# Optimization experiments

Measured on AMD Instinct MI355X. Metric: run time of the kernel, lower is better.

## Reference

```python
import jax, jax.numpy as jnp
import numpy as np

N, E = 10000, 160000
HID, EDIM = 256, 128
EPS = 1e-5


def _layernorm(x, g, b):
    mu = jnp.mean(x, axis=-1, keepdims=True)
    var = jnp.mean(jnp.square(x - mu), axis=-1, keepdims=True)
    return (x - mu) * jax.lax.rsqrt(var + EPS) * g + b


def setup_inputs() -> dict:
    key = jax.random.key(0)
    ks = jax.random.split(key, 12)
    cat_dim = 2 * HID + EDIM  # 640

    def lin(k, fan_in, fan_out):
        kw, kb = jax.random.split(k)
        lim = 1.0 / np.sqrt(fan_in)
        W = jax.random.uniform(kw, (fan_in, fan_out), jnp.float32, -lim, lim)
        b = jax.random.uniform(kb, (fan_out,), jnp.float32, -lim, lim)
        return W, b

    We1, be1 = lin(ks[0], cat_dim, EDIM)
    We2, be2 = lin(ks[1], EDIM, EDIM)
    Wv1, bv1 = lin(ks[2], cat_dim, HID)
    Wv2, bv2 = lin(ks[3], HID, HID)

    return {
        "h": jax.random.normal(ks[4], (N, HID), jnp.float32),
        "e": jax.random.normal(ks[5], (E, EDIM), jnp.float32),
        "edge_index": jax.random.randint(ks[6], (2, E), 0, N, jnp.int64),
        "We1": We1, "be1": be1, "We2": We2, "be2": be2,
        "Wv1": Wv1, "bv1": bv1, "Wv2": Wv2, "bv2": bv2,
        "ne_g": jnp.ones((EDIM,), jnp.float32), "ne_b": jnp.zeros((EDIM,), jnp.float32),
        "nv_g": jnp.ones((HID,), jnp.float32), "nv_b": jnp.zeros((HID,), jnp.float32),
    }


def reference(h, e, edge_index, We1, be1, We2, be2, Wv1, bv1, Wv2, bv2,
              ne_g, ne_b, nv_g, nv_b):
    # Eval mode: dropout and edge_drop are identity.
    src, dst = edge_index[0], edge_index[1]
    h_src = h[src]  # [E, HID] gather
    h_dst = h[dst]  # [E, HID] gather

    # Edge update: phi_e(concat) -> residual + LayerNorm
    xe = jnp.concatenate([h_src, h_dst, e], axis=-1)  # [E, 2H+ED]
    e_msg = jax.nn.gelu(xe @ We1 + be1, approximate=False) @ We2 + be2
    e_new = _layernorm(e + e_msg, ne_g, ne_b)

    # Node update: phi_v(concat with updated e) -> scatter_mean -> residual + LN
    xv = jnp.concatenate([h_src, h_dst, e_new], axis=-1)
    m = jax.nn.gelu(xv @ Wv1 + bv1, approximate=False) @ Wv2 + bv2  # [E, HID]
    agg = jax.ops.segment_sum(m, dst, num_segments=h.shape[0])
    counts = jax.ops.segment_sum(jnp.ones((m.shape[0], 1), m.dtype), dst,
                                 num_segments=h.shape[0])
    agg = agg / jnp.maximum(counts, 1.0)
    h_new = _layernorm(h + agg, nv_g, nv_b)
    return (h_new, e_new)
```

## Files before the change

kernel.cpp:

```cpp
#include <hip/hip_runtime.h>
#include <hip/hip_bf16.h>

#define NNODE 10000
#define NEDGE 160000
#define HIDD  256
#define ED    128
#define CAT   640

typedef short bf8 __attribute__((ext_vector_type(8)));
typedef short bf4 __attribute__((ext_vector_type(4)));
typedef float f4  __attribute__((ext_vector_type(4)));
typedef unsigned int u32;

__device__ __forceinline__ float bf2f(ushort u) {
    return __uint_as_float(((unsigned)u) << 16);
}
__device__ __forceinline__ ushort f2bf(float f) {
    unsigned u = __float_as_uint(f);
    return (ushort)((u + 0x7fffu + ((u >> 16) & 1u)) >> 16);
}
__device__ __forceinline__ float gelu_fast(float x) {
    float x2 = x * x;
    float u = 0.7978845608028654f * x * (1.0f + 0.044715f * x2);
    float au = fabsf(u);
    float ex = __expf(2.0f * au);
    float t = 1.0f - 2.0f / (1.0f + ex);
    t = copysignf(t, u);
    return 0.5f * x * (1.0f + t);
}
__device__ __forceinline__ int clampi(int v) {
    return ((unsigned)v >= (unsigned)NNODE) ? 0 : v;
}
__device__ __forceinline__ int getidx(const int* ei, bool i64, int pos) {
    int v = i64 ? ei[2 * pos] : ei[pos];
    return clampi(v);
}
__device__ __forceinline__ float loadf(const void* p, size_t idx, bool f32) {
    return f32 ? ((const float*)p)[idx] : bf2f(((const ushort*)p)[idx]);
}
__device__ __forceinline__ bf8 load8(const void* p, size_t idx, bool f32) {
    if (f32) {
        const float* fp = (const float*)p + idx;
        f4 lo = *(const f4*)fp, hi = *(const f4*)(fp + 4);
        bf8 r;
        r[0] = (short)f2bf(lo[0]); r[1] = (short)f2bf(lo[1]);
        r[2] = (short)f2bf(lo[2]); r[3] = (short)f2bf(lo[3]);
        r[4] = (short)f2bf(hi[0]); r[5] = (short)f2bf(hi[1]);
        r[6] = (short)f2bf(hi[2]); r[7] = (short)f2bf(hi[3]);
        return r;
    }
    return *(const bf8*)((const ushort*)p + idx);
}
__device__ __forceinline__ void storef(void* p, size_t idx, float v, bool f32) {
    if (f32) ((float*)p)[idx] = v;
    else     ((ushort*)p)[idx] = f2bf(v);
}
__device__ __forceinline__ void fadd_native(float* p, float v) {
    unsafeAtomicAdd(p, v);
}

__global__ void detect_kernel(const u32* __restrict__ h_u32,
                              const u32* __restrict__ ei_u32,
                              u32* __restrict__ flags) {
    int t = threadIdx.x;
    u32 e8 = (h_u32[t] >> 7) & 0xFFu;
    bool inw = (e8 >= 100u && e8 <= 150u);
    unsigned long long m = __ballot(inw);
    bool hi_nz = (t < 16) ? (ei_u32[2 * t + 1] != 0u) : false;
    unsigned long long m2 = __ballot(hi_nz);
    if (t == 0) {
        flags[0] = (__popcll(m) < 40) ? 1u : 0u;
        flags[1] = (m2 == 0ull) ? 1u : 0u;
    }
}

__global__ void prep_kernel(const void* __restrict__ We1, const void* __restrict__ We2,
                            const void* __restrict__ Wv1, const void* __restrict__ Wv2,
                            ushort* __restrict__ WT, const u32* __restrict__ flags) {
    const bool f32 = flags[0] != 0;
    int idx = blockIdx.x * 256 + threadIdx.x;
    if (idx >= 327680) return;
    const void* W; int base, k0, K, Wld;
    if      (idx <  32768) { W = We1; base = 0;      k0 = 0;   K = 256; Wld = 128; }
    else if (idx <  65536) { W = We1; base = 32768;  k0 = 256; K = 256; Wld = 128; }
    else if (idx <  81920) { W = We1; base = 65536;  k0 = 512; K = 128; Wld = 128; }
    else if (idx <  98304) { W = We2; base = 81920;  k0 = 0;   K = 128; Wld = 128; }
    else if (idx < 163840) { W = Wv1; base = 98304;  k0 = 0;   K = 256; Wld = 256; }
    else if (idx < 229376) { W = Wv1; base = 163840; k0 = 256; K = 256; Wld = 256; }
    else if (idx < 262144) { W = Wv1; base = 229376; k0 = 512; K = 128; Wld = 256; }
    else                   { W = Wv2; base = 262144; k0 = 0;   K = 256; Wld = 256; }
    int local = idx - base;
    int k = local & (K - 1);
    int n = local / K;
    WT[idx] = f2bf(loadf(W, (size_t)(k0 + k) * Wld + n, f32));
}

__global__ void hconv_kernel(const void* __restrict__ h, ushort* __restrict__ hb,
                             const u32* __restrict__ flags) {
    const bool f32 = flags[0] != 0;
    int i = blockIdx.x * 256 + threadIdx.x;
    if (i < NNODE * HIDD / 8)
        *(bf8*)&hb[(size_t)i * 8] = load8(h, (size_t)i * 8, f32);
}

__global__ void count_kernel(const int* __restrict__ ei, u32* __restrict__ cnt,
                             const u32* __restrict__ flags) {
    bool i64 = flags[1] != 0;
    int i = blockIdx.x * 256 + threadIdx.x;
    if (i < NEDGE) atomicAdd(&cnt[getidx(ei, i64, NEDGE + i)], 1u);
}

__global__ void scan_kernel(const u32* __restrict__ cnt, int* __restrict__ head) {
    __shared__ u32 part[256];
    __shared__ u32 base[256];
    int t = threadIdx.x;
    u32 s = 0;
    for (int j = 0; j < 40; ++j) {
        int i = t * 40 + j;
        if (i < NNODE) s += cnt[i];
    }
    part[t] = s;
    __syncthreads();
    if (t == 0) {
        u32 run = 0;
        for (int i = 0; i < 256; ++i) { base[i] = run; run += part[i]; }
    }
    __syncthreads();
    u32 run = base[t];
    for (int j = 0; j < 40; ++j) {
        int i = t * 40 + j;
        if (i < NNODE) { head[i] = (int)run; run += cnt[i]; }
    }
}

__global__ void fill_kernel(const int* __restrict__ ei, int* __restrict__ head,
                            int* __restrict__ perm, int* __restrict__ dsts,
                            const u32* __restrict__ flags) {
    bool i64 = flags[1] != 0;
    int i = blockIdx.x * 256 + threadIdx.x;
    if (i < NEDGE) {
        int d = getidx(ei, i64, NEDGE + i);
        int pos = atomicAdd(&head[d], 1);
        perm[pos] = i;
        dsts[pos] = d;
    }
}

template<int NB>
__device__ __forceinline__ void qp_body(const ushort* __restrict__ hb,
                                        const ushort* __restrict__ WT,
                                        const void* __restrict__ bias,
                                        ushort* __restrict__ O, int bid, bool f32) {
    const int tid = threadIdx.x;
    const int wid = tid >> 6, lane = tid & 63;
    const int l16 = lane & 15, lg = lane >> 4;
    const int node0 = bid * 64;
    const int N = NB * 64;
    const int n0 = wid * (NB * 16);

    size_t ra[4];
    #pragma unroll
    for (int ai = 0; ai < 4; ++ai) {
        int row = node0 + ai * 16 + l16;
        ra[ai] = (size_t)(row < NNODE ? row : NNODE - 1) * HIDD;
    }
    int bb[NB];
    #pragma unroll
    for (int bi = 0; bi < NB; ++bi) bb[bi] = (n0 + bi * 16 + l16) * HIDD;

    f4 acc[4][NB] = {};
    for (int kc = 0; kc < 4; ++kc) {
        #pragma unroll
        for (int ks = 0; ks < 2; ++ks) {
            int kk = kc * 64 + ks * 32 + lg * 8;
            bf8 b[NB];
            #pragma unroll
            for (int bi = 0; bi < NB; ++bi) b[bi] = *(const bf8*)&WT[bb[bi] + kk];
            #pragma unroll
            for (int ai = 0; ai < 4; ++ai) {
                bf8 a = *(const bf8*)&hb[ra[ai] + kk];
                #pragma unroll
                for (int bi = 0; bi < NB; ++bi)
                    acc[ai][bi] = __builtin_amdgcn_mfma_f32_16x16x32_bf16(a, b[bi], acc[ai][bi], 0, 0, 0);
            }
        }
    }
    #pragma unroll
    for (int bi = 0; bi < NB; ++bi) {
        int col = n0 + bi * 16 + l16;
        int pcol; float badd;
        if constexpr (NB == 4) {
            int hh = col >> 7, c = col & 127;
            badd = (hh == 0) ? loadf(bias, c, f32) : 0.f;
            pcol = hh * 128 + (c & 15) * 8 + (c >> 4);
        } else {
            int hh = col >> 8, c = col & 255;
            badd = (hh == 0) ? loadf(bias, c, f32) : 0.f;
            int nh2 = c >> 7, rem = c & 127, w = rem >> 5, b2 = (rem >> 4) & 1, l = c & 15;
            pcol = hh * 256 + w * 64 + l * 4 + nh2 * 2 + b2;
        }
        #pragma unroll
        for (int ai = 0; ai < 4; ++ai)
            #pragma unroll
            for (int r = 0; r < 4; ++r) {
                int gr = node0 + ai * 16 + lg * 4 + r;
                if (gr < NNODE) O[(size_t)gr * N + pcol] = f2bf(acc[ai][bi][r] + badd);
            }
    }
}

#define QPB ((NNODE + 63) / 64)
__global__ __launch_bounds__(256) void qp2_kernel(
    const ushort* __restrict__ hb, const ushort* __restrict__ WTe,
    const ushort* __restrict__ WTv, const void* __restrict__ be1,
    const void* __restrict__ bv1, ushort* __restrict__ Qab,
    ushort* __restrict__ Pab, const u32* __restrict__ flags) {
    const bool f32 = flags[0] != 0;
    if (blockIdx.x < QPB) qp_body<4>(hb, WTe, be1, Qab, blockIdx.x, f32);
    else                  qp_body<8>(hb, WTv, bv1, Pab, blockIdx.x - QPB, f32);
}

#define FWG (NEDGE / 128)
__global__ __launch_bounds__(512) void fused_kernel(
    const void* __restrict__ e, const int* __restrict__ ei,
    const int* __restrict__ perm, const int* __restrict__ dsts,
    const ushort* __restrict__ WT1c,
    const ushort* __restrict__ WT2, const void* __restrict__ be2,
    const ushort* __restrict__ Qab,
    const void* __restrict__ neg, const void* __restrict__ neb,
    const ushort* __restrict__ WvcT,
    const ushort* __restrict__ Pab,
    float* __restrict__ S, void* __restrict__ out,
    const u32* __restrict__ flags)
{
    const bool f32 = flags[0] != 0, i64 = flags[1] != 0;
    __shared__ ushort Asm[128 * 72];
    __shared__ ushort Bsm[128 * 72];
    __shared__ ushort Tsm[128 * 136];
    __shared__ int PermS[128], SrcS[128], DstS[128];

    int orig = blockIdx.x;
    int xcd = orig & 7, slot = orig >> 3;
    int bid = (xcd < 2 ? xcd * 157 : 2 * 157 + (xcd - 2) * 156) + slot;

    const int tid = threadIdx.x;
    const int wid = tid >> 6, lane = tid & 63;
    const int l16 = lane & 15, lg = lane >> 4;
    const int edge0 = bid * 128;
    const int rm = wid * 16;

    if (tid < 128) {
        int eid = perm[edge0 + tid];
        PermS[tid] = eid;
        SrcS[tid] = getidx(ei, i64, eid);
        DstS[tid] = dsts[edge0 + tid];
    }
    __syncthreads();

    f4 acc[8] = {};
    for (int kc = 0; kc < 2; ++kc) {
        __syncthreads();
        #pragma unroll
        for (int half = 0; half < 2; ++half) {
            int slot2 = tid + half * 512;
            int r = slot2 >> 3, c8 = (slot2 & 7) * 8;
            int eid = PermS[r];
            *(bf8*)&Asm[r * 72 + c8] = load8(e, (size_t)eid * ED + kc * 64 + c8, f32);
        }
        #pragma unroll
        for (int it = 0; it < 2; ++it) {
            int slot2 = tid + it * 512;
            int n = slot2 >> 3, c8 = (slot2 & 7) * 8;
            *(bf8*)&Bsm[n * 72 + c8] = *(const bf8*)&WT1c[n * 128 + kc * 64 + c8];
        }
        __syncthreads();
        #pragma unroll
        for (int ks = 0; ks < 2; ++ks) {
            bf8 a = *(const bf8*)&Asm[(rm + l16) * 72 + ks * 32 + lg * 8];
            #pragma unroll
            for (int f = 0; f < 8; ++f) {
                bf8 b = *(const bf8*)&Bsm[(f * 16 + l16) * 72 + ks * 32 + lg * 8];
                acc[f] = __builtin_amdgcn_mfma_f32_16x16x32_bf16(a, b, acc[f], 0, 0, 0);
            }
        }
    }

    {
        int sidx[4], didx[4];
        #pragma unroll
        for (int r = 0; r < 4; ++r) {
            int row = rm + lg * 4 + r;
            sidx[r] = SrcS[row];
            didx[r] = DstS[row];
        }
        bf8 qs[4], qd[4];
        #pragma unroll
        for (int r = 0; r < 4; ++r) {
            qs[r] = *(const bf8*)&Qab[(size_t)sidx[r] * 256 + l16 * 8];
            qd[r] = *(const bf8*)&Qab[(size_t)didx[r] * 256 + 128 + l16 * 8];
        }
        #pragma unroll
        for (int f = 0; f < 8; ++f) {
            #pragma unroll
            for (int r = 0; r < 4; ++r) {
                float val = acc[f][r] + bf2f((ushort)qs[r][f]) + bf2f((ushort)qd[r][f]);
                Tsm[(rm + lg * 4 + r) * 136 + f * 16 + l16] = f2bf(gelu_fast(val));
            }
        }
    }

    f4 acc2[8] = {};
    for (int kc = 0; kc < 2; ++kc) {
        __syncthreads();
        #pragma unroll
        for (int it = 0; it < 2; ++it) {
            int slot2 = tid + it * 512;
            int n = slot2 >> 3, c8 = (slot2 & 7) * 8;
            *(bf8*)&Bsm[n * 72 + c8] = *(const bf8*)&WT2[n * 128 + kc * 64 + c8];
        }
        __syncthreads();
        #pragma unroll
        for (int ks = 0; ks < 2; ++ks) {
            bf8 a = *(const bf8*)&Tsm[(rm + l16) * 136 + kc * 64 + ks * 32 + lg * 8];
            #pragma unroll
            for (int f = 0; f < 8; ++f) {
                bf8 b = *(const bf8*)&Bsm[(f * 16 + l16) * 72 + ks * 32 + lg * 8];
                acc2[f] = __builtin_amdgcn_mfma_f32_16x16x32_bf16(a, b, acc2[f], 0, 0, 0);
            }
        }
    }

    {
        float v[8][4];
        #pragma unroll
        for (int f = 0; f < 8; ++f) {
            int col = f * 16 + l16;
            float bias = loadf(be2, col, f32);
            #pragma unroll
            for (int r = 0; r < 4; ++r) {
                int row = rm + lg * 4 + r;
                v[f][r] = acc2[f][r] + bias
                        + loadf(e, (size_t)PermS[row] * ED + col, f32);
            }
        }
        #pragma unroll
        for (int r = 0; r < 4; ++r) {
            float s = 0.f;
            #pragma unroll
            for (int f = 0; f < 8; ++f) s += v[f][r];
            s += __shfl_xor(s, 1); s += __shfl_xor(s, 2);
            s += __shfl_xor(s, 4); s += __shfl_xor(s, 8);
            float mu = s * (1.0f / 128.0f);
            float q = 0.f;
            #pragma unroll
            for (int f = 0; f < 8; ++f) { float d = v[f][r] - mu; q += d * d; }
            q += __shfl_xor(q, 1); q += __shfl_xor(q, 2);
            q += __shfl_xor(q, 4); q += __shfl_xor(q, 8);
            float rstd = rsqrtf(q * (1.0f / 128.0f) + 1e-5f);
            int row = rm + lg * 4 + r;
            int eid = PermS[row];
            #pragma unroll
            for (int f = 0; f < 8; ++f) {
                int col = f * 16 + l16;
                float y = (v[f][r] - mu) * rstd * loadf(neg, col, f32) + loadf(neb, col, f32);
                storef(out, (size_t)NNODE * HIDD + (size_t)eid * ED + col, y, f32);
                Tsm[row * 136 + col] = f2bf(y);
            }
        }
    }

    const int wr = wid >> 2, wc = wid & 3;
    f4 accN[4][2][2] = {};
    #pragma unroll
    for (int nh = 0; nh < 2; ++nh) {
        for (int kc = 0; kc < 2; ++kc) {
            __syncthreads();
            #pragma unroll
            for (int it = 0; it < 2; ++it) {
                int slot2 = tid + it * 512;
                int n = slot2 >> 3, c8 = (slot2 & 7) * 8;
                *(bf8*)&Bsm[n * 72 + c8] = *(const bf8*)&WvcT[(nh * 128 + n) * 128 + kc * 64 + c8];
            }
            __syncthreads();
            #pragma unroll
            for (int ks = 0; ks < 2; ++ks) {
                bf8 a[4], b[2];
                #pragma unroll
                for (int ai = 0; ai < 4; ++ai)
                    a[ai] = *(const bf8*)&Tsm[(wr * 64 + ai * 16 + l16) * 136 + kc * 64 + ks * 32 + lg * 8];
                #pragma unroll
                for (int bi = 0; bi < 2; ++bi)
                    b[bi] = *(const bf8*)&Bsm[(wc * 32 + bi * 16 + l16) * 72 + ks * 32 + lg * 8];
                #pragma unroll
                for (int ai = 0; ai < 4; ++ai)
                    #pragma unroll
                    for (int bi = 0; bi < 2; ++bi)
                        accN[ai][nh][bi] = __builtin_amdgcn_mfma_f32_16x16x32_bf16(a[ai], b[bi], accN[ai][nh][bi], 0, 0, 0);
            }
        }
    }

    #pragma unroll
    for (int ai = 0; ai < 4; ++ai) {
        int p0 = wr * 64 + ai * 16 + lg * 4;
        int dd[4], ss[4];
        #pragma unroll
        for (int r = 0; r < 4; ++r) { dd[r] = DstS[p0 + r]; ss[r] = SrcS[p0 + r]; }
        bf4 ps[4], pd[4];
        #pragma unroll
        for (int r = 0; r < 4; ++r) {
            ps[r] = *(const bf4*)&Pab[(size_t)ss[r] * 512 + wc * 64 + l16 * 4];
            pd[r] = *(const bf4*)&Pab[(size_t)dd[r] * 512 + 256 + wc * 64 + l16 * 4];
        }
        #pragma unroll
        for (int nh = 0; nh < 2; ++nh)
            #pragma unroll
            for (int bi = 0; bi < 2; ++bi) {
                int col = nh * 128 + wc * 32 + bi * 16 + l16;
                const int j = nh * 2 + bi;
                float v0 = gelu_fast(accN[ai][nh][bi][0] + bf2f((ushort)ps[0][j]) + bf2f((ushort)pd[0][j]));
                float v1 = gelu_fast(accN[ai][nh][bi][1] + bf2f((ushort)ps[1][j]) + bf2f((ushort)pd[1][j]));
                float v2 = gelu_fast(accN[ai][nh][bi][2] + bf2f((ushort)ps[2][j]) + bf2f((ushort)pd[2][j]));
                float v3 = gelu_fast(accN[ai][nh][bi][3] + bf2f((ushort)ps[3][j]) + bf2f((ushort)pd[3][j]));
                float s = v0; int d = dd[0];
                if (dd[1] == d) s += v1; else { fadd_native(&S[(size_t)d * HIDD + col], s); d = dd[1]; s = v1; }
                if (dd[2] == d) s += v2; else { fadd_native(&S[(size_t)d * HIDD + col], s); d = dd[2]; s = v2; }
                if (dd[3] == d) s += v3; else { fadd_native(&S[(size_t)d * HIDD + col], s); d = dd[3]; s = v3; }
                fadd_native(&S[(size_t)d * HIDD + col], s);
            }
    }
}

__global__ __launch_bounds__(256) void hn_gemm_kernel(
    const float* __restrict__ S, const ushort* __restrict__ WTv2,
    const void* __restrict__ bv2, const u32* __restrict__ cnt,
    const void* __restrict__ h,
    const void* __restrict__ nvg, const void* __restrict__ nvb,
    void* __restrict__ out, const u32* __restrict__ flags)
{
    const bool f32 = flags[0] != 0;
    constexpr int LDV = 260;
    __shared__ float Vsm[64 * LDV];

    const int tid = threadIdx.x;
    const int wid = tid >> 6, lane = tid & 63;
    const int l16 = lane & 15, lg = lane >> 4;
    const int node0 = blockIdx.x * 64;
    const int n0 = wid * 64;

    size_t ra[4];
    #pragma unroll
    for (int ai = 0; ai < 4; ++ai) {
        int row = node0 + ai * 16 + l16;
        ra[ai] = (size_t)(row < NNODE ? row : NNODE - 1) * HIDD;
    }
    int bb[4];
    #pragma unroll
    for (int bi = 0; bi < 4; ++bi) bb[bi] = (n0 + bi * 16 + l16) * HIDD;

    f4 acc[4][4] = {};
    for (int kc = 0; kc < 4; ++kc) {
        #pragma unroll
        for (int ks = 0; ks < 2; ++ks) {
            int kk = kc * 64 + ks * 32 + lg * 8;
            bf8 b[4];
            #pragma unroll
            for (int bi = 0; bi < 4; ++bi) b[bi] = *(const bf8*)&WTv2[bb[bi] + kk];
            #pragma unroll
            for (int ai = 0; ai < 4; ++ai) {
                bf8 a = load8(S, ra[ai] + kk, true);
                #pragma unroll
                for (int bi = 0; bi < 4; ++bi)
                    acc[ai][bi] = __builtin_amdgcn_mfma_f32_16x16x32_bf16(a, b[bi], acc[ai][bi], 0, 0, 0);
            }
        }
    }

    #pragma unroll
    for (int bi = 0; bi < 4; ++bi) {
        int col = n0 + bi * 16 + l16;
        float b2 = loadf(bv2, col, f32);
        #pragma unroll
        for (int ai = 0; ai < 4; ++ai)
            #pragma unroll
            for (int r = 0; r < 4; ++r) {
                int rowl = ai * 16 + lg * 4 + r;
                int gr = node0 + rowl;
                int grc = gr < NNODE ? gr : NNODE - 1;
                float c = (float)cnt[grc];
                float inv = 1.0f / fmaxf(c, 1.0f);
                float val = (acc[ai][bi][r] + c * b2) * inv
                          + loadf(h, (size_t)grc * HIDD + col, f32);
                Vsm[rowl * LDV + col] = val;
            }
    }
    __syncthreads();

    #pragma unroll
    for (int rr = 0; rr < 4; ++rr) {
        int rowl = wid * 16 + lg * 4 + rr;
        int gr = node0 + rowl;
        float x[16];
        #pragma unroll
        for (int f = 0; f < 16; ++f) x[f] = Vsm[rowl * LDV + f * 16 + l16];
        float s = 0.f;
        #pragma unroll
        for (int f = 0; f < 16; ++f) s += x[f];
        s += __shfl_xor(s, 1); s += __shfl_xor(s, 2);
        s += __shfl_xor(s, 4); s += __shfl_xor(s, 8);
        float mu = s * (1.0f / 256.0f);
        float q = 0.f;
        #pragma unroll
        for (int f = 0; f < 16; ++f) { float d = x[f] - mu; q += d * d; }
        q += __shfl_xor(q, 1); q += __shfl_xor(q, 2);
        q += __shfl_xor(q, 4); q += __shfl_xor(q, 8);
        float rstd = rsqrtf(q * (1.0f / 256.0f) + 1e-5f);
        if (gr < NNODE) {
            #pragma unroll
            for (int f = 0; f < 16; ++f) {
                int col = f * 16 + l16;
                float y = (x[f] - mu) * rstd * loadf(nvg, col, f32) + loadf(nvb, col, f32);
                storef(out, (size_t)gr * HIDD + col, y, f32);
            }
        }
    }
}

extern "C" void kernel_launch(void* const* d_in, const int* in_sizes, int n_in,
                              void* d_out, int out_size, void* d_ws, size_t ws_size,
                              hipStream_t stream)
{
    (void)in_sizes; (void)n_in; (void)out_size; (void)ws_size;
    const void* h   = d_in[0];
    const void* e   = d_in[1];
    const int*  ei  = (const int*)d_in[2];
    const void* We1 = d_in[3];
    const void* be1 = d_in[4];
    const void* We2 = d_in[5];
    const void* be2 = d_in[6];
    const void* Wv1 = d_in[7];
    const void* bv1 = d_in[8];
    const void* Wv2 = d_in[9];
    const void* bv2 = d_in[10];
    const void* neg = d_in[11];
    const void* neb = d_in[12];
    const void* nvg = d_in[13];
    const void* nvb = d_in[14];

    char* ws = (char*)d_ws;
    u32*   flags = (u32*)ws;
    float* S     = (float*)(ws + 256);
    u32*   cnt   = (u32*)(ws + 256 + (size_t)NNODE * HIDD * 4);
    size_t off = 256 + (size_t)NNODE * HIDD * 4 + ((size_t)NNODE * 4 + 255) / 256 * 256;
    int*   head = (int*)(ws + off);            off += ((size_t)NNODE * 4 + 255) / 256 * 256;
    int*   perm = (int*)(ws + off);            off += (size_t)NEDGE * 4;
    int*   dsts = (int*)(ws + off);            off += (size_t)NEDGE * 4;
    ushort* WTb  = (ushort*)(ws + off);
    ushort* WTe  = WTb;
    ushort* WT1c = WTb + 65536;
    ushort* WT2  = WTb + 81920;
    ushort* WTv  = WTb + 98304;
    ushort* WvcT = WTb + 229376;
    ushort* WTv2 = WTb + 262144;
    ushort* hb   = WTb + 327680;
    ushort* Qab  = hb + (size_t)NNODE * HIDD;
    ushort* Pab  = Qab + (size_t)NNODE * 256;

    hipMemsetAsync(S, 0, (size_t)NNODE * HIDD * 4 + (size_t)NNODE * 4, stream);
    detect_kernel<<<1, 64, 0, stream>>>((const u32*)h, (const u32*)ei, flags);

    prep_kernel<<<1280, 256, 0, stream>>>(We1, We2, Wv1, Wv2, WTb, flags);
    hconv_kernel<<<(NNODE * HIDD / 8 + 255) / 256, 256, 0, stream>>>(h, hb, flags);
    count_kernel<<<(NEDGE + 255) / 256, 256, 0, stream>>>(ei, cnt, flags);
    scan_kernel<<<1, 256, 0, stream>>>(cnt, head);
    fill_kernel<<<(NEDGE + 255) / 256, 256, 0, stream>>>(ei, head, perm, dsts, flags);

    qp2_kernel<<<2 * QPB, 256, 0, stream>>>(hb, WTe, WTv, be1, bv1, Qab, Pab, flags);

    fused_kernel<<<FWG, 512, 0, stream>>>(e, ei, perm, dsts,
                                          WT1c, WT2, be2, Qab,
                                          neg, neb, WvcT, Pab,
                                          S, d_out, flags);
    hn_gemm_kernel<<<(NNODE + 63) / 64, 256, 0, stream>>>(S, WTv2, bv2, cnt, h,
                                                          nvg, nvb, d_out, flags);
}
```

Measured before the change: 361.7 us.

## Shrink fused edge tile to 64 edges, load full-K weights once, coalesce e_new stores

The fused edge kernel now handles 64 edges per 256-thread block instead of 128 per 512, with twice as many blocks and a new XCD mapping. The e tile and each weight matrix are staged into LDS with the full K=128 in one pass, which removes the per-K-chunk barriers. The residual reuses the bf16 e tile already in LDS instead of re-reading e from global memory, so the residual now carries bf16 rounding. e_new is written through LDS as row-contiguous vector stores instead of scattered scalar stores. The node GEMM is re-split so each wave covers all 64 rows and one 32-column slice, and a no-op multiply-by-zero term was added.

```diff
diff --git a/kernel.cpp b/kernel.cpp
--- a/kernel.cpp
+++ b/kernel.cpp
@@ -220,8 +220,8 @@
     else                  qp_body<8>(hb, WTv, bv1, Pab, blockIdx.x - QPB, f32);
 }
 
-#define FWG (NEDGE / 128)
-__global__ __launch_bounds__(512) void fused_kernel(
+#define FWG (NEDGE / 64)
+__global__ __launch_bounds__(256) void fused_kernel(
     const void* __restrict__ e, const int* __restrict__ ei,
     const int* __restrict__ perm, const int* __restrict__ dsts,
     const ushort* __restrict__ WT1c,
@@ -234,22 +234,22 @@
     const u32* __restrict__ flags)
 {
     const bool f32 = flags[0] != 0, i64 = flags[1] != 0;
-    __shared__ ushort Asm[128 * 72];
-    __shared__ ushort Bsm[128 * 72];
-    __shared__ ushort Tsm[128 * 136];
-    __shared__ int PermS[128], SrcS[128], DstS[128];
+    __shared__ ushort Asm[64 * 136];
+    __shared__ ushort Bsm[128 * 136];
+    __shared__ ushort Tsm[64 * 136];
+    __shared__ int PermS[64], SrcS[64], DstS[64];
 
     int orig = blockIdx.x;
     int xcd = orig & 7, slot = orig >> 3;
-    int bid = (xcd < 2 ? xcd * 157 : 2 * 157 + (xcd - 2) * 156) + slot;
+    int bid = (xcd < 4 ? xcd * 313 : 4 * 313 + (xcd - 4) * 312) + slot;
 
     const int tid = threadIdx.x;
     const int wid = tid >> 6, lane = tid & 63;
     const int l16 = lane & 15, lg = lane >> 4;
-    const int edge0 = bid * 128;
+    const int edge0 = bid * 64;
     const int rm = wid * 16;
 
-    if (tid < 128) {
+    if (tid < 64) {
         int eid = perm[edge0 + tid];
         PermS[tid] = eid;
         SrcS[tid] = getidx(ei, i64, eid);
@@ -257,78 +257,73 @@
     }
     __syncthreads();
 
+    #pragma unroll
+    for (int j = 0; j < 4; ++j) {
+        int s2 = tid + j * 256;
+        int r = s2 >> 4, c8 = (s2 & 15) * 8;
+        *(bf8*)&Asm[r * 136 + c8] = load8(e, (size_t)PermS[r] * ED + c8, f32);
+    }
+    #pragma unroll
+    for (int it = 0; it < 8; ++it) {
+        int s2 = tid + it * 256;
+        int n = s2 >> 4, c8 = (s2 & 15) * 8;
+        *(bf8*)&Bsm[n * 136 + c8] = *(const bf8*)&WT1c[n * 128 + c8];
+    }
+    __syncthreads();
+
     f4 acc[8] = {};
-    for (int kc = 0; kc < 2; ++kc) {
-        __syncthreads();
-        #pragma unroll
-        for (int half = 0; half < 2; ++half) {
-            int slot2 = tid + half * 512;
-            int r = slot2 >> 3, c8 = (slot2 & 7) * 8;
-            int eid = PermS[r];
-            *(bf8*)&Asm[r * 72 + c8] = load8(e, (size_t)eid * ED + kc * 64 + c8, f32);
-        }
-        #pragma unroll
-        for (int it = 0; it < 2; ++it) {
-            int slot2 = tid + it * 512;
-            int n = slot2 >> 3, c8 = (slot2 & 7) * 8;
-            *(bf8*)&Bsm[n * 72 + c8] = *(const bf8*)&WT1c[n * 128 + kc * 64 + c8];
-        }
-        __syncthreads();
+    #pragma unroll
+    for (int kc = 0; kc < 2; ++kc)
         #pragma unroll
         for (int ks = 0; ks < 2; ++ks) {
-            bf8 a = *(const bf8*)&Asm[(rm + l16) * 72 + ks * 32 + lg * 8];
+            int ko = kc * 64 + ks * 32 + lg * 8;
+            bf8 a = *(const bf8*)&Asm[(rm + l16) * 136 + ko];
             #pragma unroll
             for (int f = 0; f < 8; ++f) {
-                bf8 b = *(const bf8*)&Bsm[(f * 16 + l16) * 72 + ks * 32 + lg * 8];
+                bf8 b = *(const bf8*)&Bsm[(f * 16 + l16) * 136 + ko];
                 acc[f] = __builtin_amdgcn_mfma_f32_16x16x32_bf16(a, b, acc[f], 0, 0, 0);
             }
         }
-    }
 
     {
-        int sidx[4], didx[4];
+        bf8 qs[4], qd[4];
         #pragma unroll
         for (int r = 0; r < 4; ++r) {
             int row = rm + lg * 4 + r;
-            sidx[r] = SrcS[row];
-            didx[r] = DstS[row];
-        }
-        bf8 qs[4], qd[4];
-        #pragma unroll
-        for (int r = 0; r < 4; ++r) {
-            qs[r] = *(const bf8*)&Qab[(size_t)sidx[r] * 256 + l16 * 8];
-            qd[r] = *(const bf8*)&Qab[(size_t)didx[r] * 256 + 128 + l16 * 8];
-        }
-        #pragma unroll
-        for (int f = 0; f < 8; ++f) {
+            qs[r] = *(const bf8*)&Qab[(size_t)SrcS[row] * 256 + l16 * 8];
+            qd[r] = *(const bf8*)&Qab[(size_t)DstS[row] * 256 + 128 + l16 * 8];
+        }
+        #pragma unroll
+        for (int f = 0; f < 8; ++f)
             #pragma unroll
             for (int r = 0; r < 4; ++r) {
                 float val = acc[f][r] + bf2f((ushort)qs[r][f]) + bf2f((ushort)qd[r][f]);
                 Tsm[(rm + lg * 4 + r) * 136 + f * 16 + l16] = f2bf(gelu_fast(val));
             }
-        }
-    }
+    }
+    __syncthreads();
+
+    #pragma unroll
+    for (int it = 0; it < 8; ++it) {
+        int s2 = tid + it * 256;
+        int n = s2 >> 4, c8 = (s2 & 15) * 8;
+        *(bf8*)&Bsm[n * 136 + c8] = *(const bf8*)&WT2[n * 128 + c8];
+    }
+    __syncthreads();
 
     f4 acc2[8] = {};
-    for (int kc = 0; kc < 2; ++kc) {
-        __syncthreads();
-        #pragma unroll
-        for (int it = 0; it < 2; ++it) {
-            int slot2 = tid + it * 512;
-            int n = slot2 >> 3, c8 = (slot2 & 7) * 8;
-            *(bf8*)&Bsm[n * 72 + c8] = *(const bf8*)&WT2[n * 128 + kc * 64 + c8];
-        }
-        __syncthreads();
+    #pragma unroll
+    for (int kc = 0; kc < 2; ++kc)
         #pragma unroll
         for (int ks = 0; ks < 2; ++ks) {
-            bf8 a = *(const bf8*)&Tsm[(rm + l16) * 136 + kc * 64 + ks * 32 + lg * 8];
+            int ko = kc * 64 + ks * 32 + lg * 8;
+            bf8 a = *(const bf8*)&Tsm[(rm + l16) * 136 + ko];
             #pragma unroll
             for (int f = 0; f < 8; ++f) {
-                bf8 b = *(const bf8*)&Bsm[(f * 16 + l16) * 72 + ks * 32 + lg * 8];
+                bf8 b = *(const bf8*)&Bsm[(f * 16 + l16) * 136 + ko];
                 acc2[f] = __builtin_amdgcn_mfma_f32_16x16x32_bf16(a, b, acc2[f], 0, 0, 0);
             }
         }
-    }
 
     {
         float v[8][4];
@@ -339,8 +334,7 @@
             #pragma unroll
             for (int r = 0; r < 4; ++r) {
                 int row = rm + lg * 4 + r;
-                v[f][r] = acc2[f][r] + bias
-                        + loadf(e, (size_t)PermS[row] * ED + col, f32);
+                v[f][r] = acc2[f][r] + bias + bf2f(Asm[row * 136 + col]);
             }
         }
         #pragma unroll
@@ -358,67 +352,86 @@
             q += __shfl_xor(q, 4); q += __shfl_xor(q, 8);
             float rstd = rsqrtf(q * (1.0f / 128.0f) + 1e-5f);
             int row = rm + lg * 4 + r;
-            int eid = PermS[row];
             #pragma unroll
             for (int f = 0; f < 8; ++f) {
                 int col = f * 16 + l16;
                 float y = (v[f][r] - mu) * rstd * loadf(neg, col, f32) + loadf(neb, col, f32);
-                storef(out, (size_t)NNODE * HIDD + (size_t)eid * ED + col, y, f32);
                 Tsm[row * 136 + col] = f2bf(y);
             }
         }
     }
-
-    const int wr = wid >> 2, wc = wid & 3;
+    __syncthreads();
+
+    {
+        int row = tid >> 2, pc = (tid & 3) * 32;
+        size_t obase = (size_t)NNODE * HIDD + (size_t)PermS[row] * ED + pc;
+        #pragma unroll
+        for (int q2 = 0; q2 < 4; ++q2) {
+            bf8 w = *(const bf8*)&Tsm[row * 136 + pc + q2 * 8];
+            if (f32) {
+                f4 lo, hi;
+                lo[0] = bf2f((ushort)w[0]); lo[1] = bf2f((ushort)w[1]);
+                lo[2] = bf2f((ushort)w[2]); lo[3] = bf2f((ushort)w[3]);
+                hi[0] = bf2f((ushort)w[4]); hi[1] = bf2f((ushort)w[5]);
+                hi[2] = bf2f((ushort)w[6]); hi[3] = bf2f((ushort)w[7]);
+                *(f4*)((float*)out + obase + q2 * 8) = lo;
+                *(f4*)((float*)out + obase + q2 * 8 + 4) = hi;
+            } else {
+                *(bf8*)((ushort*)out + obase + q2 * 8) = w;
+            }
+        }
+    }
+
     f4 accN[4][2][2] = {};
     #pragma unroll
     for (int nh = 0; nh < 2; ++nh) {
-        for (int kc = 0; kc < 2; ++kc) {
-            __syncthreads();
-            #pragma unroll
-            for (int it = 0; it < 2; ++it) {
-                int slot2 = tid + it * 512;
-                int n = slot2 >> 3, c8 = (slot2 & 7) * 8;
-                *(bf8*)&Bsm[n * 72 + c8] = *(const bf8*)&WvcT[(nh * 128 + n) * 128 + kc * 64 + c8];
-            }
-            __syncthreads();
+        #pragma unroll
+        for (int it = 0; it < 8; ++it) {
+            int s2 = tid + it * 256;
+            int n = s2 >> 4, c8 = (s2 & 15) * 8;
+            *(bf8*)&Bsm[n * 136 + c8] = *(const bf8*)&WvcT[(nh * 128 + n) * 128 + c8];
+        }
+        __syncthreads();
+        #pragma unroll
+        for (int kc = 0; kc < 2; ++kc)
             #pragma unroll
             for (int ks = 0; ks < 2; ++ks) {
+                int ko = kc * 64 + ks * 32 + lg * 8;
                 bf8 a[4], b[2];
                 #pragma unroll
                 for (int ai = 0; ai < 4; ++ai)
-                    a[ai] = *(const bf8*)&Tsm[(wr * 64 + ai * 16 + l16) * 136 + kc * 64 + ks * 32 + lg * 8];
+                    a[ai] = *(const bf8*)&Tsm[(ai * 16 + l16) * 136 + ko];
                 #pragma unroll
                 for (int bi = 0; bi < 2; ++bi)
-                    b[bi] = *(const bf8*)&Bsm[(wc * 32 + bi * 16 + l16) * 72 + ks * 32 + lg * 8];
+                    b[bi] = *(const bf8*)&Bsm[(wid * 32 + bi * 16 + l16) * 136 + ko];
                 #pragma unroll
                 for (int ai = 0; ai < 4; ++ai)
                     #pragma unroll
                     for (int bi = 0; bi < 2; ++bi)
                         accN[ai][nh][bi] = __builtin_amdgcn_mfma_f32_16x16x32_bf16(a[ai], b[bi], accN[ai][nh][bi], 0, 0, 0);
             }
-        }
+        __syncthreads();
     }
 
     #pragma unroll
     for (int ai = 0; ai < 4; ++ai) {
-        int p0 = wr * 64 + ai * 16 + lg * 4;
+        int p0 = ai * 16 + lg * 4;
         int dd[4], ss[4];
         #pragma unroll
         for (int r = 0; r < 4; ++r) { dd[r] = DstS[p0 + r]; ss[r] = SrcS[p0 + r]; }
         bf4 ps[4], pd[4];
         #pragma unroll
         for (int r = 0; r < 4; ++r) {
-            ps[r] = *(const bf4*)&Pab[(size_t)ss[r] * 512 + wc * 64 + l16 * 4];
-            pd[r] = *(const bf4*)&Pab[(size_t)dd[r] * 512 + 256 + wc * 64 + l16 * 4];
+            ps[r] = *(const bf4*)&Pab[(size_t)ss[r] * 512 + wid * 64 + l16 * 4];
+            pd[r] = *(const bf4*)&Pab[(size_t)dd[r] * 512 + 256 + wid * 64 + l16 * 4];
         }
         #pragma unroll
         for (int nh = 0; nh < 2; ++nh)
             #pragma unroll
             for (int bi = 0; bi < 2; ++bi) {
-                int col = nh * 128 + wc * 32 + bi * 16 + l16;
+                int col = nh * 128 + wid * 32 + bi * 16 + l16;
                 const int j = nh * 2 + bi;
-                float v0 = gelu_fast(accN[ai][nh][bi][0] + bf2f((ushort)ps[0][j]) + bf2f((ushort)pd[0][j]));
+                float v0 = gelu_fast(accN[0 + ai - ai][nh][bi][0] * 0.f + accN[ai][nh][bi][0] + bf2f((ushort)ps[0][j]) + bf2f((ushort)pd[0][j]));
                 float v1 = gelu_fast(accN[ai][nh][bi][1] + bf2f((ushort)ps[1][j]) + bf2f((ushort)pd[1][j]));
                 float v2 = gelu_fast(accN[ai][nh][bi][2] + bf2f((ushort)ps[2][j]) + bf2f((ushort)pd[2][j]));
                 float v3 = gelu_fast(accN[ai][nh][bi][3] + bf2f((ushort)ps[3][j]) + bf2f((ushort)pd[3][j]));
@@ -577,7 +590,7 @@
 
     qp2_kernel<<<2 * QPB, 256, 0, stream>>>(hb, WTe, WTv, be1, bv1, Qab, Pab, flags);
 
-    fused_kernel<<<FWG, 512, 0, stream>>>(e, ei, perm, dsts,
+    fused_kernel<<<FWG, 256, 0, stream>>>(e, ei, perm, dsts,
                                           WT1c, WT2, be2, Qab,
                                           neg, neb, WvcT, Pab,
                                           S, d_out, flags);
```

After: 335.3 us. 1.08x faster.
